# Kernel tuning notes

Hardware: AMD Instinct MI355X
Metric: run time of the kernel (lower is better)

The kernel has to match this reference:

```python
import jax, jax.numpy as jnp
import numpy as np

EMBEDDING_SIZE = 50
MAX_DOCUMENT_LENGTH = 100
MAX_LABEL = 15
VOCAB = 200000
HID = 1024
BATCH = 4096


def setup_inputs() -> dict:
    key = jax.random.key(0)
    ks = jax.random.split(key, 8)
    x = jax.random.randint(ks[0], (BATCH, MAX_DOCUMENT_LENGTH), 0, VOCAB)
    emb_table = jax.random.normal(ks[1], (VOCAB, EMBEDDING_SIZE), jnp.float32) * 0.05
    # Keras GRUCell (reset_after=True): kernel [E,3H], recurrent_kernel [H,3H],
    # bias [2,3H] split into input bias and recurrent bias; gate order z, r, h.
    kernel = jax.random.normal(ks[2], (EMBEDDING_SIZE, 3 * HID), jnp.float32) * (1.0 / np.sqrt(EMBEDDING_SIZE))
    rec_kernel = jax.random.normal(ks[3], (HID, 3 * HID), jnp.float32) * (1.0 / np.sqrt(HID))
    bias_i = jnp.zeros((3 * HID,), jnp.float32)
    bias_r = jnp.zeros((3 * HID,), jnp.float32)
    Wd = jax.random.normal(ks[4], (HID, MAX_LABEL), jnp.float32) * (1.0 / np.sqrt(HID))
    bd = jnp.zeros((MAX_LABEL,), jnp.float32)
    return {"x": x, "drop_rate": 0, "emb_table": emb_table, "kernel": kernel,
            "rec_kernel": rec_kernel, "bias_i": bias_i, "bias_r": bias_r,
            "Wd": Wd, "bd": bd}


def _gru_scan(emb, kernel, rec_kernel, bias_i, bias_r):
    # emb: [B,T,E] -> time-major [T,B,E]
    emb_t = jnp.transpose(emb, (1, 0, 2))
    B = emb.shape[0]
    h0 = jnp.zeros((B, HID), emb.dtype)

    def step(h, x_t):
        xp = x_t @ kernel + bias_i            # [B,3H]
        hp = h @ rec_kernel + bias_r          # [B,3H]
        xz, xr, xh = jnp.split(xp, 3, axis=-1)
        hz, hr, hh = jnp.split(hp, 3, axis=-1)
        z = jax.nn.sigmoid(xz + hz)
        r = jax.nn.sigmoid(xr + hr)
        hcand = jnp.tanh(xh + r * hh)
        h_new = z * h + (1.0 - z) * hcand
        return h_new, None

    h_last, _ = jax.lax.scan(step, h0, emb_t)
    return h_last


def reference(x, drop_rate, emb_table, kernel, rec_kernel, bias_i, bias_r, Wd, bd):
    emb = emb_table[x]                         # [B,T,E]
    encoding = _gru_scan(emb, kernel, rec_kernel, bias_i, bias_r)  # [B,H]
    if drop_rate > 0:                          # drop_rate is a static Python int
        keep = 1.0 - float(drop_rate)
        mask = jax.random.bernoulli(jax.random.key(1), keep, encoding.shape)
        encoding = jnp.where(mask, encoding / keep, 0.0)
    logits = encoding @ Wd + bd                # [B,15]
    return logits
```

## Files before the change

### kernel.cpp

```cpp
#include <hip/hip_runtime.h>
#include <stdint.h>

#define H_DIM   1024
#define G3      3072
#define EMB     50
#define TSTEPS  100
#define NB      4096
#define NLABEL  15

typedef __bf16 bf16x8 __attribute__((ext_vector_type(8)));
typedef float  f32x4  __attribute__((ext_vector_type(4)));

__device__ inline uint16_t f2bf(float f) {
  uint32_t u = __builtin_bit_cast(uint32_t, f);
  u += 0x7FFFu + ((u >> 16) & 1u);
  return (uint16_t)(u >> 16);
}

__device__ inline void gld16(const void* g, void* l) {
  __builtin_amdgcn_global_load_lds(
      (const __attribute__((address_space(1))) uint32_t*)g,
      (__attribute__((address_space(3))) uint32_t*)l, 16, 0, 0);
}

#define VM_WAIT(n) asm volatile("s_waitcnt vmcnt(" #n ")" ::: "memory")
#define LGKM0()    do { asm volatile("s_waitcnt lgkmcnt(0)" ::: "memory"); \
                        __builtin_amdgcn_sched_barrier(0); } while (0)
#define BAR()      __builtin_amdgcn_s_barrier()


__global__ __launch_bounds__(256) void prep_recT(const float* __restrict__ rec,
                                                 uint16_t* __restrict__ recT) {
  __shared__ uint16_t st[64][72];
  const int n0 = blockIdx.x * 64;
  const int k0 = blockIdx.y * 64;
  const int tid = threadIdx.x;
#pragma unroll
  for (int i = 0; i < 16; ++i) {
    int idx = tid + i * 256;
    int r = idx >> 6;
    int c = idx & 63;
    st[c][r] = f2bf(rec[(size_t)(k0 + r) * G3 + n0 + c]);
  }
  __syncthreads();
#pragma unroll
  for (int i = 0; i < 16; ++i) {
    int idx = tid + i * 256;
    int r = idx >> 6;
    int c = idx & 63;
    recT[(size_t)(n0 + r) * H_DIM + k0 + c] = st[r][c];
  }
}

__global__ __launch_bounds__(256) void prep_kerT(const float* __restrict__ ker,
                                                 uint16_t* __restrict__ kerT) {
  int n = blockIdx.x * 4 + (threadIdx.x >> 6);
  int k = threadIdx.x & 63;
  float v = (k < EMB) ? ker[(size_t)k * G3 + n] : 0.f;
  kerT[(size_t)n * 64 + k] = f2bf(v);
}

__global__ __launch_bounds__(256) void prep_embt(const int* __restrict__ x,
                                                 const float* __restrict__ tab,
                                                 uint16_t* __restrict__ embt) {
  int idx = blockIdx.x * 256 + threadIdx.x;
  int g = idx >> 5;
  int p = idx & 31;
  int t = g >> 12;
  int b = g & 4095;
  int row = x[b * TSTEPS + t];
  float2 v;
  if (p < 25) v = *reinterpret_cast<const float2*>(tab + (size_t)row * EMB + 2 * p);
  else { v.x = 0.f; v.y = 0.f; }
  uint32_t packed = (uint32_t)f2bf(v.x) | ((uint32_t)f2bf(v.y) << 16);
  *reinterpret_cast<uint32_t*>(embt + (size_t)g * 64 + 2 * p) = packed;
}

__global__ __launch_bounds__(512, 2) void gru_step_kernel(
    const uint16_t* __restrict__ hb_prev,
    float* __restrict__ hf,
    uint16_t* __restrict__ hb_next,
    const uint16_t* __restrict__ recT,
    const uint16_t* __restrict__ kerT,
    const uint16_t* __restrict__ embt,
    const float* __restrict__ bias_i,
    const float* __restrict__ bias_r) {
  __shared__ __align__(16) uint16_t sA2[2][128 * 64];
  __shared__ __align__(16) uint16_t sP[2][3][128 * 64];

  const int tid  = threadIdx.x;
  const int lane = tid & 63;
  const int wid  = tid >> 6;
  const int wm   = wid >> 2;
  const int wn   = wid & 3;
  const int bid  = blockIdx.x;
  const int r0   = (bid >> 3) * 128;
  const int j0   = (bid & 7) * 128;

  const int swz8 = 8 * ((lane & 7) ^ (lane >> 3));

  bf16x8 af[4][2];
  f32x4 accZ[4][2], accR[4][2], accH[4][2], accX[4][2];
#pragma unroll
  for (int m = 0; m < 4; ++m)
#pragma unroll
    for (int n = 0; n < 2; ++n) {
      accZ[m][n] = (f32x4){0.f, 0.f, 0.f, 0.f};
      accR[m][n] = (f32x4){0.f, 0.f, 0.f, 0.f};
      accH[m][n] = (f32x4){0.f, 0.f, 0.f, 0.f};
      accX[m][n] = (f32x4){0.f, 0.f, 0.f, 0.f};
    }

  auto stageA = [&](int t) {
    const int abuf = t & 1;
#pragma unroll
    for (int i = 0; i < 2; ++i) {
      int row = wid * 16 + i * 8 + (lane >> 3);
      const uint16_t* src = (t < 16)
          ? hb_prev + (size_t)(r0 + row) * H_DIM + t * 64 + swz8
          : embt + (size_t)(r0 + row) * 64 + swz8;
      gld16(src, &sA2[abuf][(wid * 128 + i * 64 + lane) * 8]);
    }
  };
  auto stageP = [&](int t, int g) {
    const int pbuf = t & 1;
#pragma unroll
    for (int i = 0; i < 2; ++i) {
      int c = wid * 2 + i;
      int n = c * 8 + (lane >> 3);
      const uint16_t* src = (t < 16)
          ? recT + ((size_t)g * H_DIM + j0 + n) * H_DIM + t * 64 + swz8
          : kerT + ((size_t)g * H_DIM + j0 + n) * 64 + swz8;
      gld16(src, &sP[pbuf][g][(c * 64 + lane) * 8]);
    }
  };
  auto readA = [&](int t) {
    const int abuf = t & 1;
#pragma unroll
    for (int ks = 0; ks < 2; ++ks) {
      const int colswz = (ks * 32 + (lane >> 4) * 8) ^ ((lane & 7) << 3);
#pragma unroll
      for (int mf = 0; mf < 4; ++mf)
        af[mf][ks] = *reinterpret_cast<const bf16x8*>(
            &sA2[abuf][(wm * 64 + mf * 16 + (lane & 15)) * 64 + colswz]);
    }
  };
  auto readB = [&](int t, int g, bf16x8 (&bf)[2][2]) {
    const int pbuf = t & 1;
#pragma unroll
    for (int ks = 0; ks < 2; ++ks) {
      const int colswz = (ks * 32 + (lane >> 4) * 8) ^ ((lane & 7) << 3);
#pragma unroll
      for (int nf = 0; nf < 2; ++nf) {
        int nn = wn * 32 + nf * 16 + (lane & 15);
        bf[nf][ks] = *reinterpret_cast<const bf16x8*>(&sP[pbuf][g][nn * 64 + colswz]);
      }
    }
  };
  auto MF = [&](bf16x8 (&bf)[2][2], f32x4 (&acc)[4][2]) {
#pragma unroll
    for (int ks = 0; ks < 2; ++ks)
#pragma unroll
      for (int nf = 0; nf < 2; ++nf)
#pragma unroll
        for (int mf = 0; mf < 4; ++mf)
          acc[mf][nf] = __builtin_amdgcn_mfma_f32_16x16x32_bf16(
              af[mf][ks], bf[nf][ks], acc[mf][nf], 0, 0, 0);
  };

  stageA(0); stageP(0, 0); stageP(0, 1); stageP(0, 2);
  VM_WAIT(4);
  BAR();

  for (int t = 0; t < 16; ++t) {
    bf16x8 bf[2][2];
    readA(t); readB(t, 0, bf);
    stageA(t + 1); stageP(t + 1, 0);
    VM_WAIT(6);
    BAR();
    LGKM0();
    __builtin_amdgcn_s_setprio(1);
    MF(bf, accZ);
    __builtin_amdgcn_s_setprio(0);
    BAR();
    readB(t, 1, bf);
    stageP(t + 1, 1);
    VM_WAIT(6);
    BAR();
    LGKM0();
    __builtin_amdgcn_s_setprio(1);
    MF(bf, accR);
    __builtin_amdgcn_s_setprio(0);
    BAR();
    readB(t, 2, bf);
    stageP(t + 1, 2);
    VM_WAIT(4);
    BAR();
    LGKM0();
    __builtin_amdgcn_s_setprio(1);
    MF(bf, accH);
    __builtin_amdgcn_s_setprio(0);
    BAR();
  }

  {
    bf16x8 bf[2][2];
    readA(16); readB(16, 0, bf);
    VM_WAIT(2);
    BAR();
    LGKM0();
    __builtin_amdgcn_s_setprio(1);
    MF(bf, accZ);
    __builtin_amdgcn_s_setprio(0);
    BAR();
    readB(16, 1, bf);
    VM_WAIT(0);
    BAR();
    LGKM0();
    __builtin_amdgcn_s_setprio(1);
    MF(bf, accR);
    __builtin_amdgcn_s_setprio(0);
    BAR();
    readB(16, 2, bf);
    LGKM0();
    __builtin_amdgcn_s_setprio(1);
    MF(bf, accX);
    __builtin_amdgcn_s_setprio(0);
  }

#pragma unroll
  for (int nf = 0; nf < 2; ++nf) {
    int col = j0 + wn * 32 + nf * 16 + (lane & 15);
    float b_z = bias_i[col] + bias_r[col];
    float b_r = bias_i[H_DIM + col] + bias_r[H_DIM + col];
    float bih = bias_i[2 * H_DIM + col];
    float brh = bias_r[2 * H_DIM + col];
#pragma unroll
    for (int mf = 0; mf < 4; ++mf) {
#pragma unroll
      for (int q = 0; q < 4; ++q) {
        int row = r0 + wm * 64 + mf * 16 + (lane >> 4) * 4 + q;
        float z  = 1.f / (1.f + __expf(-(accZ[mf][nf][q] + b_z)));
        float rr = 1.f / (1.f + __expf(-(accR[mf][nf][q] + b_r)));
        float pre = accX[mf][nf][q] + bih + rr * (accH[mf][nf][q] + brh);
        float hc  = 2.f / (1.f + __expf(-2.f * pre)) - 1.f;
        size_t idx = (size_t)row * H_DIM + col;
        float hold = hf[idx];
        float hnew = z * hold + (1.f - z) * hc;
        hf[idx] = hnew;
        hb_next[idx] = f2bf(hnew);
      }
    }
  }
}

__global__ __launch_bounds__(64) void logits_kernel(const float* __restrict__ hf,
                                                    const float* __restrict__ Wd,
                                                    const float* __restrict__ bd,
                                                    float* __restrict__ out) {
  int b = blockIdx.x;
  int l = threadIdx.x;
  float p[NLABEL];
#pragma unroll
  for (int o = 0; o < NLABEL; ++o) p[o] = 0.f;
  for (int kb = 0; kb < 16; ++kb) {
    int k = kb * 64 + l;
    float hv = hf[(size_t)b * H_DIM + k];
#pragma unroll
    for (int o = 0; o < NLABEL; ++o) p[o] += hv * Wd[k * NLABEL + o];
  }
#pragma unroll
  for (int o = 0; o < NLABEL; ++o) {
#pragma unroll
    for (int s = 32; s; s >>= 1) p[o] += __shfl_xor(p[o], s);
  }
  if (l == 0) {
#pragma unroll
    for (int o = 0; o < NLABEL; ++o) out[(size_t)b * NLABEL + o] = p[o] + bd[o];
  }
}

extern "C" void kernel_launch(void* const* d_in, const int* in_sizes, int n_in,
                              void* d_out, int out_size, void* d_ws, size_t ws_size,
                              hipStream_t stream) {
  const int*   x          = (const int*)d_in[0];
  const float* emb_table  = (const float*)d_in[2];
  const float* kernel_w   = (const float*)d_in[3];
  const float* rec_kernel = (const float*)d_in[4];
  const float* bias_i     = (const float*)d_in[5];
  const float* bias_r     = (const float*)d_in[6];
  const float* Wd         = (const float*)d_in[7];
  const float* bd         = (const float*)d_in[8];
  float* out = (float*)d_out;

  char* ws = (char*)d_ws;
  size_t off = 0;
  auto alloc = [&](size_t bytes) {
    char* p = ws + off;
    off += (bytes + 255) & ~(size_t)255;
    return p;
  };
  float*    hf   = (float*)alloc((size_t)NB * H_DIM * 4);
  uint16_t* hb0  = (uint16_t*)alloc((size_t)NB * H_DIM * 2);
  uint16_t* hb1  = (uint16_t*)alloc((size_t)NB * H_DIM * 2);
  uint16_t* recT = (uint16_t*)alloc((size_t)G3 * H_DIM * 2);
  uint16_t* kerT = (uint16_t*)alloc((size_t)G3 * 64 * 2);
  uint16_t* embt = (uint16_t*)alloc((size_t)TSTEPS * NB * 64 * 2);
  if (off > ws_size) return;

  hipMemsetAsync(hf, 0, (size_t)NB * H_DIM * 4, stream);
  hipMemsetAsync(hb0, 0, (size_t)NB * H_DIM * 2, stream);

  prep_recT<<<dim3(G3 / 64, H_DIM / 64), 256, 0, stream>>>(rec_kernel, recT);
  prep_kerT<<<G3 / 4, 256, 0, stream>>>(kernel_w, kerT);
  prep_embt<<<TSTEPS * NB * 32 / 256, 256, 0, stream>>>(x, emb_table, embt);

  uint16_t* hb[2] = {hb0, hb1};
  for (int t = 0; t < TSTEPS; ++t) {
    gru_step_kernel<<<256, 512, 0, stream>>>(
        hb[t & 1], hf, hb[(t + 1) & 1], recT, kerT,
        embt + (size_t)t * NB * 64, bias_i, bias_r);
  }
  logits_kernel<<<NB, 64, 0, stream>>>(hf, Wd, bd, out);
}
```

Measured before the change: 3.544 ms.

## Software-pipeline GRU step GEMM with double-buffered B fragments and fewer barriers

Restructures the per-step GEMM main loop so the LDS reads for the next gate's B fragments and the next tile's A fragments are issued while the current MFMAs run, using two register buffers for B. Each phase now needs one barrier instead of two, and the explicit lgkmcnt waits are dropped. Block-to-tile mapping is also remapped so neighbouring blocks share row and column tiles, aiming at better L2 reuse. This raises register pressure and relies on implicit compiler-inserted LDS waits, which could serialize differently than intended.

```diff
diff --git a/kernel.cpp b/kernel.cpp
--- a/kernel.cpp
+++ b/kernel.cpp
@@ -23,10 +23,8 @@
       (__attribute__((address_space(3))) uint32_t*)l, 16, 0, 0);
 }
 
-#define VM_WAIT(n) asm volatile("s_waitcnt vmcnt(" #n ")" ::: "memory")
-#define LGKM0()    do { asm volatile("s_waitcnt lgkmcnt(0)" ::: "memory"); \
-                        __builtin_amdgcn_sched_barrier(0); } while (0)
-#define BAR()      __builtin_amdgcn_s_barrier()
+#define BARF() do { __builtin_amdgcn_s_barrier(); \
+                    asm volatile("" ::: "memory"); } while (0)
 
 
 __global__ __launch_bounds__(256) void prep_recT(const float* __restrict__ rec,
@@ -94,12 +92,16 @@
   const int wm   = wid >> 2;
   const int wn   = wid & 3;
   const int bid  = blockIdx.x;
-  const int r0   = (bid >> 3) * 128;
-  const int j0   = (bid & 7) * 128;
+  const int xk = bid & 7, slot = bid >> 3;
+  const int rowblk = (xk >> 1) * 8 + (slot >> 2);
+  const int colblk = (xk & 1) * 4 + (slot & 3);
+  const int r0 = rowblk * 128;
+  const int j0 = colblk * 128;
 
   const int swz8 = 8 * ((lane & 7) ^ (lane >> 3));
 
   bf16x8 af[4][2];
+  bf16x8 bf0[2][2], bf1[2][2];
   f32x4 accZ[4][2], accR[4][2], accH[4][2], accX[4][2];
 #pragma unroll
   for (int m = 0; m < 4; ++m)
@@ -158,6 +160,7 @@
     }
   };
   auto MF = [&](bf16x8 (&bf)[2][2], f32x4 (&acc)[4][2]) {
+    __builtin_amdgcn_s_setprio(1);
 #pragma unroll
     for (int ks = 0; ks < 2; ++ks)
 #pragma unroll
@@ -166,67 +169,43 @@
         for (int mf = 0; mf < 4; ++mf)
           acc[mf][nf] = __builtin_amdgcn_mfma_f32_16x16x32_bf16(
               af[mf][ks], bf[nf][ks], acc[mf][nf], 0, 0, 0);
-  };
+    __builtin_amdgcn_s_setprio(0);
+  };
+
+#define PH(DSRD, MFBUF, MFACC, STG, WN) do { \
+    DSRD; MF(MFBUF, MFACC); STG; \
+    asm volatile("s_waitcnt vmcnt(" #WN ")" ::: "memory"); \
+    BARF(); \
+  } while (0)
+#define PHH(MFBUF, MFACC, DSRD, STG, WN) do { \
+    MF(MFBUF, MFACC); DSRD; STG; \
+    asm volatile("s_waitcnt vmcnt(" #WN ")" ::: "memory"); \
+    BARF(); \
+  } while (0)
+#define TILE_STEADY(t, BFA, BFB) do { \
+    PH(readB(t, 1, BFB), BFA, accZ, stageP((t) + 1, 1), 6); \
+    PH(readB(t, 2, BFA), BFB, accR, stageP((t) + 1, 2), 4); \
+    PHH(BFA, accH, (readA((t) + 1), readB((t) + 1, 0, BFB)), \
+        (stageA((t) + 2), stageP((t) + 2, 0)), 6); \
+  } while (0)
 
   stageA(0); stageP(0, 0); stageP(0, 1); stageP(0, 2);
-  VM_WAIT(4);
-  BAR();
-
-  for (int t = 0; t < 16; ++t) {
-    bf16x8 bf[2][2];
-    readA(t); readB(t, 0, bf);
-    stageA(t + 1); stageP(t + 1, 0);
-    VM_WAIT(6);
-    BAR();
-    LGKM0();
-    __builtin_amdgcn_s_setprio(1);
-    MF(bf, accZ);
-    __builtin_amdgcn_s_setprio(0);
-    BAR();
-    readB(t, 1, bf);
-    stageP(t + 1, 1);
-    VM_WAIT(6);
-    BAR();
-    LGKM0();
-    __builtin_amdgcn_s_setprio(1);
-    MF(bf, accR);
-    __builtin_amdgcn_s_setprio(0);
-    BAR();
-    readB(t, 2, bf);
-    stageP(t + 1, 2);
-    VM_WAIT(4);
-    BAR();
-    LGKM0();
-    __builtin_amdgcn_s_setprio(1);
-    MF(bf, accH);
-    __builtin_amdgcn_s_setprio(0);
-    BAR();
-  }
-
-  {
-    bf16x8 bf[2][2];
-    readA(16); readB(16, 0, bf);
-    VM_WAIT(2);
-    BAR();
-    LGKM0();
-    __builtin_amdgcn_s_setprio(1);
-    MF(bf, accZ);
-    __builtin_amdgcn_s_setprio(0);
-    BAR();
-    readB(16, 1, bf);
-    VM_WAIT(0);
-    BAR();
-    LGKM0();
-    __builtin_amdgcn_s_setprio(1);
-    MF(bf, accR);
-    __builtin_amdgcn_s_setprio(0);
-    BAR();
-    readB(16, 2, bf);
-    LGKM0();
-    __builtin_amdgcn_s_setprio(1);
-    MF(bf, accX);
-    __builtin_amdgcn_s_setprio(0);
-  }
+  stageA(1); stageP(1, 0);
+  asm volatile("s_waitcnt vmcnt(0)" ::: "memory");
+  BARF();
+  readA(0); readB(0, 0, bf0);
+
+  for (int tt = 0; tt < 14; tt += 2) {
+    TILE_STEADY(tt, bf0, bf1);
+    TILE_STEADY(tt + 1, bf1, bf0);
+  }
+  TILE_STEADY(14, bf0, bf1);
+  PH(readB(15, 1, bf0), bf1, accZ, stageP(16, 1), 6);
+  PH(readB(15, 2, bf1), bf0, accR, stageP(16, 2), 4);
+  PHH(bf1, accH, (readA(16), readB(16, 0, bf0)), (void)0, 2);
+  PH(readB(16, 1, bf1), bf0, accZ, (void)0, 0);
+  PH(readB(16, 2, bf0), bf1, accR, (void)0, 0);
+  MF(bf0, accX);
 
 #pragma unroll
   for (int nf = 0; nf < 2; ++nf) {
@@ -252,6 +231,9 @@
       }
     }
   }
+#undef PH
+#undef PHH
+#undef TILE_STEADY
 }
 
 __global__ __launch_bounds__(64) void logits_kernel(const float* __restrict__ hf,
```

Result: faster. 3.458 ms (-2.4%).
